# Kernel optimization log

Hardware: AMD Instinct MI355X
Metric: run time of the kernel (lower is better)

Reference implementation:

```python
import jax, jax.numpy as jnp
import numpy as np

USER_NUM = 80000
ITEM_NUM = 40000
N = USER_NUM + ITEM_NUM
EMB = 64
NNZ = 1200000
N_LAYERS = 3


def setup_inputs() -> dict:
    key = jax.random.key(0)
    k1, k2, k3, k4, k5 = jax.random.split(key, 5)
    # xavier_uniform bound for [num, emb]
    bu = float(np.sqrt(6.0 / (USER_NUM + EMB)))
    bi = float(np.sqrt(6.0 / (ITEM_NUM + EMB)))
    user_emb = jax.random.uniform(k1, (USER_NUM, EMB), jnp.float32, -bu, bu)
    item_emb = jax.random.uniform(k2, (ITEM_NUM, EMB), jnp.float32, -bi, bi)
    adj_rows = jax.random.randint(k3, (NNZ,), 0, N, dtype=jnp.int32)
    adj_cols = jax.random.randint(k4, (NNZ,), 0, N, dtype=jnp.int32)
    # normalized-adjacency-like positive values
    adj_vals = jax.random.uniform(k5, (NNZ,), jnp.float32) * (1.0 / 32.0)
    return {"user_emb": user_emb, "item_emb": item_emb,
            "adj_vals": adj_vals, "adj_rows": adj_rows, "adj_cols": adj_cols}


def _spmm(vals, rows, cols, x):
    # out[r] = sum_{e: rows[e]==r} vals[e] * x[cols[e]]   (COO SpMM)
    return jax.ops.segment_sum(vals[:, None] * x[cols], rows, num_segments=N)


def reference(user_emb, item_emb, adj_vals, adj_rows, adj_cols):
    ego = jnp.concatenate([user_emb, item_emb], axis=0)  # [N, d]
    acc = jnp.zeros_like(ego)
    for _ in range(N_LAYERS):
        ego = _spmm(adj_vals, adj_rows, adj_cols, ego)
        acc = acc + ego
    all_emb = acc / N_LAYERS  # mean over stacked layer outputs
    user_all = all_emb[:USER_NUM]
    item_all = all_emb[USER_NUM:]
    return (user_all, item_all)
```

## Files before the change

### kernel.cpp

```cpp
#include <hip/hip_runtime.h>
#include <hip/hip_fp16.h>

#define USER_NUM 80000
#define ITEM_NUM 40000
#define NNODE (USER_NUM + ITEM_NUM)
#define EMB 64
#define NB 469
#define P1_CHUNK 4096

#define HSCALE 8192.0f
#define HINV   (1.0f / 8192.0f)

#define CONV_ITEMS (NNODE * EMB / 8)
#define CONV_BLOCKS ((CONV_ITEMS + 255) / 256)

__global__ void convhist_kernel(const float* __restrict__ ue, const float* __restrict__ ie,
                                ushort* __restrict__ x0h,
                                const int* __restrict__ rows, int* __restrict__ bcounts,
                                int nnz) {
    __shared__ int h[NB];
    if (blockIdx.x < 256) {
        for (int i = threadIdx.x; i < NB; i += 256) h[i] = 0;
        __syncthreads();
        int nq = nnz >> 2;
        int stride = 256 * 256;
        for (int i = blockIdx.x * 256 + threadIdx.x; i < nq; i += stride) {
            int4 r = ((const int4*)rows)[i];
            atomicAdd(&h[r.x >> 8], 1);
            atomicAdd(&h[r.y >> 8], 1);
            atomicAdd(&h[r.z >> 8], 1);
            atomicAdd(&h[r.w >> 8], 1);
        }
        if (blockIdx.x == 0) {
            for (int i = (nq << 2) + threadIdx.x; i < nnz; i += 256)
                atomicAdd(&h[rows[i] >> 8], 1);
        }
        __syncthreads();
        for (int i = threadIdx.x; i < NB; i += 256)
            if (h[i]) atomicAdd(&bcounts[i], h[i]);
    } else {
        int idx = (blockIdx.x - 256) * 256 + threadIdx.x;
        if (idx >= CONV_ITEMS) return;
        const int utotal = USER_NUM * EMB / 8;
        const float4* src = (idx < utotal) ? ((const float4*)ue) + 2 * (size_t)idx
                                           : ((const float4*)ie) + 2 * (size_t)(idx - utotal);
        float4 a = src[0], b = src[1];
        __half2 h0 = __floats2half2_rn(a.x * HSCALE, a.y * HSCALE);
        __half2 h1 = __floats2half2_rn(a.z * HSCALE, a.w * HSCALE);
        __half2 h2 = __floats2half2_rn(b.x * HSCALE, b.y * HSCALE);
        __half2 h3 = __floats2half2_rn(b.z * HSCALE, b.w * HSCALE);
        uint4 pk = make_uint4(*(const unsigned*)&h0, *(const unsigned*)&h1,
                              *(const unsigned*)&h2, *(const unsigned*)&h3);
        ((uint4*)x0h)[idx] = pk;
    }
}

__global__ void bucket_scan_kernel(const int* __restrict__ bcounts, int* __restrict__ bucket_off,
                                   int* __restrict__ bcursor, int* __restrict__ row_ptr, int nnz) {
    __shared__ int lds[512];
    int t = threadIdx.x;
    int v = (t < NB) ? bcounts[t] : 0;
    lds[t] = v;
    __syncthreads();
    for (int off = 1; off < 512; off <<= 1) {
        int add = (t >= off) ? lds[t - off] : 0;
        __syncthreads();
        lds[t] += add;
        __syncthreads();
    }
    if (t < NB) {
        int ex = lds[t] - v;
        bucket_off[t] = ex;
        bcursor[t]    = ex;
    }
    if (t == 0) { bucket_off[NB] = nnz; row_ptr[NNODE] = nnz; }
}

__global__ void phase1_kernel(const int* __restrict__ rows, const int* __restrict__ cols,
                              const float* __restrict__ vals, int* __restrict__ bcursor,
                              int2* __restrict__ tmp, int nnz) {
    __shared__ int h[NB];
    __shared__ int base[NB];
    int t = threadIdx.x;
    for (int i = t; i < NB; i += 256) h[i] = 0;
    __syncthreads();
    int lo = blockIdx.x * P1_CHUNK;
    int hi = lo + P1_CHUNK; if (hi > nnz) hi = nnz;
    int n4 = (hi - lo) >> 2;
    const int4*   rows4 = (const int4*)(rows + lo);
    const int4*   cols4 = (const int4*)(cols + lo);
    const float4* vals4 = (const float4*)(vals + lo);

    for (int i = t; i < n4; i += 256) {
        int4 r = rows4[i];
        atomicAdd(&h[r.x >> 8], 1);
        atomicAdd(&h[r.y >> 8], 1);
        atomicAdd(&h[r.z >> 8], 1);
        atomicAdd(&h[r.w >> 8], 1);
    }
    for (int i = lo + (n4 << 2) + t; i < hi; i += 256)
        atomicAdd(&h[rows[i] >> 8], 1);
    __syncthreads();
    for (int i = t; i < NB; i += 256) {
        int c = h[i];
        base[i] = c ? atomicAdd(&bcursor[i], c) : 0;
        h[i] = 0;
    }
    __syncthreads();
    for (int i = t; i < n4; i += 256) {
        int4 r = rows4[i];
        int4 c = cols4[i];
        float4 v = vals4[i];
        {
            int b = r.x >> 8; int loc = atomicAdd(&h[b], 1);
            tmp[base[b] + loc] = make_int2(c.x | ((r.x & 255) << 17), __float_as_int(v.x));
        }
        {
            int b = r.y >> 8; int loc = atomicAdd(&h[b], 1);
            tmp[base[b] + loc] = make_int2(c.y | ((r.y & 255) << 17), __float_as_int(v.y));
        }
        {
            int b = r.z >> 8; int loc = atomicAdd(&h[b], 1);
            tmp[base[b] + loc] = make_int2(c.z | ((r.z & 255) << 17), __float_as_int(v.z));
        }
        {
            int b = r.w >> 8; int loc = atomicAdd(&h[b], 1);
            tmp[base[b] + loc] = make_int2(c.w | ((r.w & 255) << 17), __float_as_int(v.w));
        }
    }
    for (int i = lo + (n4 << 2) + t; i < hi; i += 256) {
        int r = rows[i];
        int b = r >> 8;
        int loc = atomicAdd(&h[b], 1);
        tmp[base[b] + loc] = make_int2(cols[i] | ((r & 255) << 17), __float_as_int(vals[i]));
    }
}

__global__ void phase2_kernel(const int2* __restrict__ tmp, const int* __restrict__ bucket_off,
                              int* __restrict__ row_ptr, int2* __restrict__ edges) {
    __shared__ int hist[256];
    __shared__ int scan[256];
    __shared__ int cur[256];
    int b = blockIdx.x;
    int t = threadIdx.x;
    int row0  = b << 8;
    int nrows = NNODE - row0; if (nrows > 256) nrows = 256;
    int start = bucket_off[b];
    int end   = bucket_off[b + 1];
    if (t < 256) hist[t] = 0;
    __syncthreads();
    for (int j = start + t; j < end; j += 1024)
        atomicAdd(&hist[tmp[j].x >> 17], 1);
    __syncthreads();
    int v = 0;
    if (t < 256) { v = hist[t]; scan[t] = v; }
    __syncthreads();
    for (int off = 1; off < 256; off <<= 1) {
        int add = 0;
        if (t < 256 && t >= off) add = scan[t - off];
        __syncthreads();
        if (t < 256) scan[t] += add;
        __syncthreads();
    }
    if (t < 256) {
        int ex = scan[t] - v + start;
        if (t < nrows) row_ptr[row0 + t] = ex;
        cur[t] = ex;
    }
    __syncthreads();
    for (int j = start + t; j < end; j += 1024) {
        int2 e  = tmp[j];
        int rl  = e.x >> 17;
        int pos = atomicAdd(&cur[rl], 1);
        edges[pos] = make_int2(e.x & 0x1FFFF, e.y);
    }
}

__device__ __forceinline__ float4 unpack_half4(uint2 gv) {
    float2 a = __half22float2(*(const __half2*)&gv.x);
    float2 b = __half22float2(*(const __half2*)&gv.y);
    return make_float4(a.x, a.y, b.x, b.y);
}

template <bool FINAL>
__launch_bounds__(256)
__global__ void spmm_kernel(const ushort* __restrict__ xh,
                            const int* __restrict__ row_ptr, const int2* __restrict__ edges,
                            ushort* __restrict__ yh,
                            const ushort* __restrict__ y1h_own, float* __restrict__ out) {
    int wave = (blockIdx.x * blockDim.x + threadIdx.x) >> 6;
    int lane = threadIdx.x & 63;
    int r0 = wave << 3;
    if (r0 >= NNODE) return;
    int g = lane >> 3;
    int c = lane & 7;

    int rp = 0;
    if (lane < 9) rp = row_ptr[r0 + lane];
    int p0 = __builtin_amdgcn_readlane(rp, 0);
    int p1 = __builtin_amdgcn_readlane(rp, 1);
    int p2 = __builtin_amdgcn_readlane(rp, 2);
    int p3 = __builtin_amdgcn_readlane(rp, 3);
    int p4 = __builtin_amdgcn_readlane(rp, 4);
    int p5 = __builtin_amdgcn_readlane(rp, 5);
    int p6 = __builtin_amdgcn_readlane(rp, 6);
    int p7 = __builtin_amdgcn_readlane(rp, 7);
    int p8 = __builtin_amdgcn_readlane(rp, 8);

    int sg = (g < 4) ? ((g < 2) ? (g == 0 ? p0 : p1) : (g == 2 ? p2 : p3))
                     : ((g < 6) ? (g == 4 ? p4 : p5) : (g == 6 ? p6 : p7));
    int eg = (g < 4) ? ((g < 2) ? (g == 0 ? p1 : p2) : (g == 2 ? p3 : p4))
                     : ((g < 6) ? (g == 4 ? p5 : p6) : (g == 6 ? p7 : p8));
    int maxd = max(max(max(p1 - p0, p2 - p1), max(p3 - p2, p4 - p3)),
                   max(max(p5 - p4, p6 - p5), max(p7 - p6, p8 - p7)));

    float4 acc0 = make_float4(0.f, 0.f, 0.f, 0.f);
    float4 acc1 = make_float4(0.f, 0.f, 0.f, 0.f);

    for (int j = 0; j < maxd; j += 8) {
        long long ev[8];
        #pragma unroll
        for (int u = 0; u < 8; ++u) {
            int i = sg + j + u;
            ev[u] = (i < eg) ? *(const long long*)(edges + i) : 0LL;
        }
        #pragma unroll
        for (int u = 0; u < 8; ++u) {
            int   col = (int)(unsigned)ev[u];
            float v   = __int_as_float((int)(ev[u] >> 32));
            uint4 hv = ((const uint4*)(xh + (size_t)col * EMB))[c];
            float2 a0 = __half22float2(*(const __half2*)&hv.x);
            float2 a1 = __half22float2(*(const __half2*)&hv.y);
            float2 a2 = __half22float2(*(const __half2*)&hv.z);
            float2 a3 = __half22float2(*(const __half2*)&hv.w);
            acc0.x += v * a0.x; acc0.y += v * a0.y;
            acc0.z += v * a1.x; acc0.w += v * a1.y;
            acc1.x += v * a2.x; acc1.y += v * a2.y;
            acc1.z += v * a3.x; acc1.w += v * a3.y;
        }
    }

    int row = r0 + g;
    size_t oh = (size_t)row * EMB + (size_t)c * 8;

    if (!FINAL) {
        __half2 h0 = __floats2half2_rn(acc0.x, acc0.y);
        __half2 h1 = __floats2half2_rn(acc0.z, acc0.w);
        __half2 h2 = __floats2half2_rn(acc1.x, acc1.y);
        __half2 h3 = __floats2half2_rn(acc1.z, acc1.w);
        uint4 pk = make_uint4(*(const unsigned*)&h0, *(const unsigned*)&h1,
                              *(const unsigned*)&h2, *(const unsigned*)&h3);
        *(uint4*)(yh + oh) = pk;
    } else {
        uint4 o1 = *(const uint4*)(y1h_own + oh);
        uint4 o2 = *(const uint4*)(xh + oh);
        float4 y1a = unpack_half4(make_uint2(o1.x, o1.y));
        float4 y1b = unpack_half4(make_uint2(o1.z, o1.w));
        float4 y2a = unpack_half4(make_uint2(o2.x, o2.y));
        float4 y2b = unpack_half4(make_uint2(o2.z, o2.w));
        const float s = HINV / 3.0f;
        float4 ta, tb;
        ta.x = (y1a.x + y2a.x + acc0.x) * s;
        ta.y = (y1a.y + y2a.y + acc0.y) * s;
        ta.z = (y1a.z + y2a.z + acc0.z) * s;
        ta.w = (y1a.w + y2a.w + acc0.w) * s;
        tb.x = (y1b.x + y2b.x + acc1.x) * s;
        tb.y = (y1b.y + y2b.y + acc1.y) * s;
        tb.z = (y1b.z + y2b.z + acc1.z) * s;
        tb.w = (y1b.w + y2b.w + acc1.w) * s;
        *(float4*)(out + oh)     = ta;
        *(float4*)(out + oh + 4) = tb;
    }
}

__global__ void init_kernel(const float* __restrict__ user_emb, const float* __restrict__ item_emb,
                            float* __restrict__ x, float* __restrict__ out) {
    int idx = blockIdx.x * blockDim.x + threadIdx.x;
    const int total = NNODE * EMB / 4;
    if (idx >= total) return;
    const int user_total = USER_NUM * EMB / 4;
    float4 v = (idx < user_total) ? ((const float4*)user_emb)[idx]
                                  : ((const float4*)item_emb)[idx - user_total];
    ((float4*)x)[idx]   = v;
    ((float4*)out)[idx] = make_float4(0.f, 0.f, 0.f, 0.f);
}

__global__ void scatter_kernel(const float* __restrict__ x, float* __restrict__ y,
                               const float* __restrict__ vals, const int* __restrict__ rows,
                               const int* __restrict__ cols, int nnz) {
    int tid = blockIdx.x * blockDim.x + threadIdx.x;
    int e = tid >> 4;
    if (e >= nnz) return;
    int c = tid & 15;
    int r = rows[e], col = cols[e];
    float v = vals[e];
    float4 xv = ((const float4*)(x + (size_t)col * EMB))[c];
    float* dst = y + (size_t)r * EMB + (size_t)c * 4;
    atomicAdd(dst + 0, xv.x * v);
    atomicAdd(dst + 1, xv.y * v);
    atomicAdd(dst + 2, xv.z * v);
    atomicAdd(dst + 3, xv.w * v);
}

__global__ void accum_kernel(float* __restrict__ out, const float* __restrict__ y, float scale) {
    int idx = blockIdx.x * blockDim.x + threadIdx.x;
    const int total = NNODE * EMB / 4;
    if (idx >= total) return;
    float4 o = ((float4*)out)[idx];
    float4 a = ((const float4*)y)[idx];
    o.x = (o.x + a.x) * scale; o.y = (o.y + a.y) * scale;
    o.z = (o.z + a.z) * scale; o.w = (o.w + a.w) * scale;
    ((float4*)out)[idx] = o;
}

extern "C" void kernel_launch(void* const* d_in, const int* in_sizes, int n_in,
                              void* d_out, int out_size, void* d_ws, size_t ws_size,
                              hipStream_t stream) {
    const float* user_emb = (const float*)d_in[0];
    const float* item_emb = (const float*)d_in[1];
    const float* vals     = (const float*)d_in[2];
    const int*   rows     = (const int*)d_in[3];
    const int*   cols     = (const int*)d_in[4];
    const int    nnz      = in_sizes[2];

    float* out = (float*)d_out;

    const size_t embN   = (size_t)NNODE * EMB;
    const size_t rp_pad = 120064;

    size_t need = (2 * embN + rp_pad) * 4 + (size_t)nnz * 8;

    if (ws_size >= need) {
        float* bufA    = (float*)d_ws;
        float* bufB    = bufA + embN;
        int*   row_ptr = (int*)(bufB + embN);
        int2*  edges   = (int2*)(row_ptr + rp_pad);

        int2* tmp        = (int2*)bufA;
        int*  bcounts    = (int*)bufB;
        int*  bucket_off = bcounts + 512;
        int*  bcursor    = bucket_off + 512;

        ushort* y1h = (ushort*)bufA;
        ushort* y2h = y1h + embN;
        ushort* x0h = ((ushort*)bufB) + embN;

        hipMemsetAsync(bcounts, 0, NB * sizeof(int), stream);
        convhist_kernel<<<256 + CONV_BLOCKS, 256, 0, stream>>>(user_emb, item_emb, x0h,
                                                               rows, bcounts, nnz);
        bucket_scan_kernel<<<1, 512, 0, stream>>>(bcounts, bucket_off, bcursor, row_ptr, nnz);
        phase1_kernel<<<(nnz + P1_CHUNK - 1) / P1_CHUNK, 256, 0, stream>>>(rows, cols, vals, bcursor, tmp, nnz);
        phase2_kernel<<<NB, 1024, 0, stream>>>(tmp, bucket_off, row_ptr, edges);

        const int nwaves = NNODE / 8;
        const int blocks = (nwaves * 64 + 255) / 256;
        spmm_kernel<false><<<blocks, 256, 0, stream>>>(x0h, row_ptr, edges, y1h, nullptr, nullptr);
        spmm_kernel<false><<<blocks, 256, 0, stream>>>(y1h, row_ptr, edges, y2h, nullptr, nullptr);
        spmm_kernel<true ><<<blocks, 256, 0, stream>>>(y2h, row_ptr, edges, nullptr, y1h, out);
    } else {
        float* x = (float*)d_ws;
        float* y = x + embN;
        const size_t emb_bytes = embN * sizeof(float);
        {
            int total = NNODE * EMB / 4;
            init_kernel<<<(total + 255) / 256, 256, 0, stream>>>(user_emb, item_emb, x, out);
        }
        for (int layer = 0; layer < 3; ++layer) {
            hipMemsetAsync(y, 0, emb_bytes, stream);
            long long threads = (long long)nnz * 16;
            scatter_kernel<<<(int)((threads + 255) / 256), 256, 0, stream>>>(x, y, vals, rows, cols, nnz);
            int total = NNODE * EMB / 4;
            accum_kernel<<<(total + 255) / 256, 256, 0, stream>>>(out, y, layer < 2 ? 1.0f : (1.0f / 3.0f));
            float* t = x; x = y; y = t;
        }
    }
}
```

Measured before the change: 212.1 us.

## Replace two-pass bucket sort CSR build with global per-row atomic counting sort

```diff
diff --git a/kernel.cpp b/kernel.cpp
--- a/kernel.cpp
+++ b/kernel.cpp
@@ -5,41 +5,35 @@
 #define ITEM_NUM 40000
 #define NNODE (USER_NUM + ITEM_NUM)
 #define EMB 64
-#define NB 469
-#define P1_CHUNK 4096
+#define SC_CHUNK 4096
 
 #define HSCALE 8192.0f
 #define HINV   (1.0f / 8192.0f)
 
+#define HIST_BLOCKS 1024
 #define CONV_ITEMS (NNODE * EMB / 8)
 #define CONV_BLOCKS ((CONV_ITEMS + 255) / 256)
 
-__global__ void convhist_kernel(const float* __restrict__ ue, const float* __restrict__ ie,
-                                ushort* __restrict__ x0h,
-                                const int* __restrict__ rows, int* __restrict__ bcounts,
-                                int nnz) {
-    __shared__ int h[NB];
-    if (blockIdx.x < 256) {
-        for (int i = threadIdx.x; i < NB; i += 256) h[i] = 0;
-        __syncthreads();
+__global__ void convrowhist_kernel(const float* __restrict__ ue, const float* __restrict__ ie,
+                                   ushort* __restrict__ x0h,
+                                   const int* __restrict__ rows, int* __restrict__ rcount,
+                                   int nnz) {
+    if (blockIdx.x < HIST_BLOCKS) {
         int nq = nnz >> 2;
-        int stride = 256 * 256;
+        int stride = HIST_BLOCKS * 256;
         for (int i = blockIdx.x * 256 + threadIdx.x; i < nq; i += stride) {
             int4 r = ((const int4*)rows)[i];
-            atomicAdd(&h[r.x >> 8], 1);
-            atomicAdd(&h[r.y >> 8], 1);
-            atomicAdd(&h[r.z >> 8], 1);
-            atomicAdd(&h[r.w >> 8], 1);
+            atomicAdd(&rcount[r.x], 1);
+            atomicAdd(&rcount[r.y], 1);
+            atomicAdd(&rcount[r.z], 1);
+            atomicAdd(&rcount[r.w], 1);
         }
         if (blockIdx.x == 0) {
             for (int i = (nq << 2) + threadIdx.x; i < nnz; i += 256)
-                atomicAdd(&h[rows[i] >> 8], 1);
-        }
-        __syncthreads();
-        for (int i = threadIdx.x; i < NB; i += 256)
-            if (h[i]) atomicAdd(&bcounts[i], h[i]);
+                atomicAdd(&rcount[rows[i]], 1);
+        }
     } else {
-        int idx = (blockIdx.x - 256) * 256 + threadIdx.x;
+        int idx = (blockIdx.x - HIST_BLOCKS) * 256 + threadIdx.x;
         if (idx >= CONV_ITEMS) return;
         const int utotal = USER_NUM * EMB / 8;
         const float4* src = (idx < utotal) ? ((const float4*)ue) + 2 * (size_t)idx
@@ -55,37 +49,38 @@
     }
 }
 
-__global__ void bucket_scan_kernel(const int* __restrict__ bcounts, int* __restrict__ bucket_off,
-                                   int* __restrict__ bcursor, int* __restrict__ row_ptr, int nnz) {
-    __shared__ int lds[512];
+__global__ void rowscan_kernel(const int* __restrict__ rcount, int* __restrict__ row_ptr,
+                               int* __restrict__ cursor, int nnz) {
+    __shared__ int lds[1024];
     int t = threadIdx.x;
-    int v = (t < NB) ? bcounts[t] : 0;
-    lds[t] = v;
+    const int CHUNK = (NNODE + 1023) / 1024;
+    int lo = t * CHUNK;
+    int hi = lo + CHUNK; if (hi > NNODE) hi = NNODE;
+    int s = 0;
+    for (int i = lo; i < hi; ++i) s += rcount[i];
+    lds[t] = s;
     __syncthreads();
-    for (int off = 1; off < 512; off <<= 1) {
+    for (int off = 1; off < 1024; off <<= 1) {
         int add = (t >= off) ? lds[t - off] : 0;
         __syncthreads();
         lds[t] += add;
         __syncthreads();
     }
-    if (t < NB) {
-        int ex = lds[t] - v;
-        bucket_off[t] = ex;
-        bcursor[t]    = ex;
-    }
-    if (t == 0) { bucket_off[NB] = nnz; row_ptr[NNODE] = nnz; }
-}
-
-__global__ void phase1_kernel(const int* __restrict__ rows, const int* __restrict__ cols,
-                              const float* __restrict__ vals, int* __restrict__ bcursor,
-                              int2* __restrict__ tmp, int nnz) {
-    __shared__ int h[NB];
-    __shared__ int base[NB];
+    int run = lds[t] - s;
+    for (int i = lo; i < hi; ++i) {
+        row_ptr[i] = run;
+        cursor[i]  = run;
+        run += rcount[i];
+    }
+    if (t == 1023) row_ptr[NNODE] = nnz;
+}
+
+__global__ void scatter_build_kernel(const int* __restrict__ rows, const int* __restrict__ cols,
+                                     const float* __restrict__ vals, int* __restrict__ cursor,
+                                     int2* __restrict__ edges, int nnz) {
     int t = threadIdx.x;
-    for (int i = t; i < NB; i += 256) h[i] = 0;
-    __syncthreads();
-    int lo = blockIdx.x * P1_CHUNK;
-    int hi = lo + P1_CHUNK; if (hi > nnz) hi = nnz;
+    int lo = blockIdx.x * SC_CHUNK;
+    int hi = lo + SC_CHUNK; if (hi > nnz) hi = nnz;
     int n4 = (hi - lo) >> 2;
     const int4*   rows4 = (const int4*)(rows + lo);
     const int4*   cols4 = (const int4*)(cols + lo);
@@ -93,86 +88,16 @@
 
     for (int i = t; i < n4; i += 256) {
         int4 r = rows4[i];
-        atomicAdd(&h[r.x >> 8], 1);
-        atomicAdd(&h[r.y >> 8], 1);
-        atomicAdd(&h[r.z >> 8], 1);
-        atomicAdd(&h[r.w >> 8], 1);
-    }
-    for (int i = lo + (n4 << 2) + t; i < hi; i += 256)
-        atomicAdd(&h[rows[i] >> 8], 1);
-    __syncthreads();
-    for (int i = t; i < NB; i += 256) {
-        int c = h[i];
-        base[i] = c ? atomicAdd(&bcursor[i], c) : 0;
-        h[i] = 0;
-    }
-    __syncthreads();
-    for (int i = t; i < n4; i += 256) {
-        int4 r = rows4[i];
         int4 c = cols4[i];
         float4 v = vals4[i];
-        {
-            int b = r.x >> 8; int loc = atomicAdd(&h[b], 1);
-            tmp[base[b] + loc] = make_int2(c.x | ((r.x & 255) << 17), __float_as_int(v.x));
-        }
-        {
-            int b = r.y >> 8; int loc = atomicAdd(&h[b], 1);
-            tmp[base[b] + loc] = make_int2(c.y | ((r.y & 255) << 17), __float_as_int(v.y));
-        }
-        {
-            int b = r.z >> 8; int loc = atomicAdd(&h[b], 1);
-            tmp[base[b] + loc] = make_int2(c.z | ((r.z & 255) << 17), __float_as_int(v.z));
-        }
-        {
-            int b = r.w >> 8; int loc = atomicAdd(&h[b], 1);
-            tmp[base[b] + loc] = make_int2(c.w | ((r.w & 255) << 17), __float_as_int(v.w));
-        }
+        { int pos = atomicAdd(&cursor[r.x], 1); edges[pos] = make_int2(c.x, __float_as_int(v.x)); }
+        { int pos = atomicAdd(&cursor[r.y], 1); edges[pos] = make_int2(c.y, __float_as_int(v.y)); }
+        { int pos = atomicAdd(&cursor[r.z], 1); edges[pos] = make_int2(c.z, __float_as_int(v.z)); }
+        { int pos = atomicAdd(&cursor[r.w], 1); edges[pos] = make_int2(c.w, __float_as_int(v.w)); }
     }
     for (int i = lo + (n4 << 2) + t; i < hi; i += 256) {
-        int r = rows[i];
-        int b = r >> 8;
-        int loc = atomicAdd(&h[b], 1);
-        tmp[base[b] + loc] = make_int2(cols[i] | ((r & 255) << 17), __float_as_int(vals[i]));
-    }
-}
-
-__global__ void phase2_kernel(const int2* __restrict__ tmp, const int* __restrict__ bucket_off,
-                              int* __restrict__ row_ptr, int2* __restrict__ edges) {
-    __shared__ int hist[256];
-    __shared__ int scan[256];
-    __shared__ int cur[256];
-    int b = blockIdx.x;
-    int t = threadIdx.x;
-    int row0  = b << 8;
-    int nrows = NNODE - row0; if (nrows > 256) nrows = 256;
-    int start = bucket_off[b];
-    int end   = bucket_off[b + 1];
-    if (t < 256) hist[t] = 0;
-    __syncthreads();
-    for (int j = start + t; j < end; j += 1024)
-        atomicAdd(&hist[tmp[j].x >> 17], 1);
-    __syncthreads();
-    int v = 0;
-    if (t < 256) { v = hist[t]; scan[t] = v; }
-    __syncthreads();
-    for (int off = 1; off < 256; off <<= 1) {
-        int add = 0;
-        if (t < 256 && t >= off) add = scan[t - off];
-        __syncthreads();
-        if (t < 256) scan[t] += add;
-        __syncthreads();
-    }
-    if (t < 256) {
-        int ex = scan[t] - v + start;
-        if (t < nrows) row_ptr[row0 + t] = ex;
-        cur[t] = ex;
-    }
-    __syncthreads();
-    for (int j = start + t; j < end; j += 1024) {
-        int2 e  = tmp[j];
-        int rl  = e.x >> 17;
-        int pos = atomicAdd(&cur[rl], 1);
-        edges[pos] = make_int2(e.x & 0x1FFFF, e.y);
+        int pos = atomicAdd(&cursor[rows[i]], 1);
+        edges[pos] = make_int2(cols[i], __float_as_int(vals[i]));
     }
 }
 
@@ -336,21 +261,19 @@
         int*   row_ptr = (int*)(bufB + embN);
         int2*  edges   = (int2*)(row_ptr + rp_pad);
 
-        int2* tmp        = (int2*)bufA;
-        int*  bcounts    = (int*)bufB;
-        int*  bucket_off = bcounts + 512;
-        int*  bcursor    = bucket_off + 512;
+        int* rcount = (int*)bufB;
+        int* cursor = rcount + NNODE;
 
         ushort* y1h = (ushort*)bufA;
         ushort* y2h = y1h + embN;
         ushort* x0h = ((ushort*)bufB) + embN;
 
-        hipMemsetAsync(bcounts, 0, NB * sizeof(int), stream);
-        convhist_kernel<<<256 + CONV_BLOCKS, 256, 0, stream>>>(user_emb, item_emb, x0h,
-                                                               rows, bcounts, nnz);
-        bucket_scan_kernel<<<1, 512, 0, stream>>>(bcounts, bucket_off, bcursor, row_ptr, nnz);
-        phase1_kernel<<<(nnz + P1_CHUNK - 1) / P1_CHUNK, 256, 0, stream>>>(rows, cols, vals, bcursor, tmp, nnz);
-        phase2_kernel<<<NB, 1024, 0, stream>>>(tmp, bucket_off, row_ptr, edges);
+        hipMemsetAsync(rcount, 0, NNODE * sizeof(int), stream);
+        convrowhist_kernel<<<HIST_BLOCKS + CONV_BLOCKS, 256, 0, stream>>>(user_emb, item_emb, x0h,
+                                                                          rows, rcount, nnz);
+        rowscan_kernel<<<1, 1024, 0, stream>>>(rcount, row_ptr, cursor, nnz);
+        scatter_build_kernel<<<(nnz + SC_CHUNK - 1) / SC_CHUNK, 256, 0, stream>>>(rows, cols, vals,
+                                                                                  cursor, edges, nnz);
 
         const int nwaves = NNODE / 8;
         const int blocks = (nwaves * 64 + 255) / 256;
```

Result: slower. 572.0 us (+169.7%).
